# Optimization experiments

Measured on AMD Instinct MI355X. Metric: run time of the kernel, lower is better.

Reference implementation:

```python
import jax, jax.numpy as jnp
import numpy as np

HIDDEN = 2048
KEY_DIM = 2048
NUM_HEADS = 16
EPS = 1e-05


def rms_norm(x, w, eps=EPS):
    ms = jnp.mean(x * x, axis=-1, keepdims=True)
    return x * jax.lax.rsqrt(ms + eps) * w


def setup_inputs() -> dict:
    key = jax.random.key(0)
    ks = jax.random.split(key, 6)
    bound = 1.0 / np.sqrt(HIDDEN)  # kaiming-uniform-ish scale
    x = jax.random.normal(ks[0], (2, 2048, HIDDEN), dtype=jnp.float32)
    rms_w = jnp.ones((HIDDEN,), dtype=jnp.float32)
    Wq = jax.random.uniform(ks[1], (HIDDEN, KEY_DIM), jnp.float32, -bound, bound)
    Wk = jax.random.uniform(ks[2], (HIDDEN, KEY_DIM), jnp.float32, -bound, bound)
    Wv = jax.random.uniform(ks[3], (HIDDEN, KEY_DIM), jnp.float32, -bound, bound)
    Wo = jax.random.uniform(ks[4], (KEY_DIM, HIDDEN), jnp.float32, -bound, bound)
    return {"x": x, "rms_w": rms_w, "Wq": Wq, "Wk": Wk, "Wv": Wv, "Wo": Wo}


def reference(x, rms_w, Wq, Wk, Wv, Wo):
    B, S, _ = x.shape
    residual = x
    xn = rms_norm(x, rms_w)
    # project and split heads: [B,S,H,Dh]
    q = (xn @ Wq).reshape(B, S, NUM_HEADS, KEY_DIM // NUM_HEADS)
    k = (xn @ Wk).reshape(B, S, NUM_HEADS, KEY_DIM // NUM_HEADS)
    v = (xn @ Wv).reshape(B, S, NUM_HEADS, KEY_DIM // NUM_HEADS)
    # NOTE: original scales by 1/sqrt(key_dim), not head_dim — kept faithful
    scale = 1.0 / jnp.sqrt(jnp.float32(KEY_DIM))
    scores = jnp.einsum('bshd,bthd->bhst', q, k) * scale  # [B,H,S,S]
    causal = jnp.tril(jnp.ones((S, S), dtype=bool))
    scores = jnp.where(causal[None, None], scores, -jnp.inf)
    probs = jax.nn.softmax(scores, axis=-1)  # stable max-subtract internally
    out = jnp.einsum('bhst,bthd->bshd', probs, v).reshape(B, S, KEY_DIM)
    return out @ Wo + residual
```

## Files before the change

kernel.cpp:

```cpp
#include <hip/hip_runtime.h>
#include <math.h>

typedef __attribute__((ext_vector_type(8))) short bf16x8;
typedef __attribute__((ext_vector_type(4))) float f32x4;
typedef __attribute__((ext_vector_type(16))) float f32x16;

#define HID 2048
#define SEQ 2048
#define NH  16
#define DH  128
#define QS_LOG2E 0.0318793607f

__device__ __forceinline__ ushort f2bf(float f) {
  union { float f; unsigned u; } v; v.f = f;
  unsigned r = v.u + 0x7fffu + ((v.u >> 16) & 1u);
  return (ushort)(r >> 16);
}

__device__ __forceinline__ void gload16(const ushort* g, ushort* l) {
  __builtin_amdgcn_global_load_lds((const __attribute__((address_space(1))) void*)g,
                                   (__attribute__((address_space(3))) void*)l,
                                   16, 0, 0);
}

#define VMCNT(n) asm volatile("s_waitcnt vmcnt(" #n ")" ::: "memory")
#define ABAR()   asm volatile("s_barrier" ::: "memory")

__global__ __launch_bounds__(256) void k_prep(const float* __restrict__ W0,
                                              const float* __restrict__ W1,
                                              const float* __restrict__ W2,
                                              const float* __restrict__ W3,
                                              ushort* __restrict__ T0,
                                              ushort* __restrict__ T3,
                                              const float* __restrict__ x,
                                              const float* __restrict__ rw,
                                              ushort* __restrict__ xn) {
  const int z = blockIdx.z;
  if (z < 4) {
    __shared__ float t[32][33];
    const float* W = (z == 0) ? W0 : (z == 1) ? W1 : (z == 2) ? W2 : W3;
    ushort* Wt = (z == 3) ? T3 : (T0 + (size_t)z * 2048 * 2048);
    int n0 = blockIdx.x * 32, k0 = blockIdx.y * 32;
    int tx = threadIdx.x, ty = threadIdx.y;
    for (int i = ty; i < 32; i += 8)
      t[i][tx] = W[(size_t)(k0 + i) * HID + n0 + tx];
    __syncthreads();
    for (int i = ty; i < 32; i += 8)
      Wt[(size_t)(n0 + i) * HID + k0 + tx] = f2bf(t[tx][i]);
  } else {
    const int tid = threadIdx.y * 32 + threadIdx.x;
    const int row = blockIdx.y * 64 + blockIdx.x;
    const float* xr = x + (size_t)row * HID;
    int base = tid * 8;
    float4 a = *(const float4*)(xr + base);
    float4 c = *(const float4*)(xr + base + 4);
    float ss = a.x*a.x + a.y*a.y + a.z*a.z + a.w*a.w
             + c.x*c.x + c.y*c.y + c.z*c.z + c.w*c.w;
    #pragma unroll
    for (int off = 32; off > 0; off >>= 1) ss += __shfl_xor(ss, off);
    __shared__ float red[4];
    if ((tid & 63) == 0) red[tid >> 6] = ss;
    __syncthreads();
    float tot = red[0] + red[1] + red[2] + red[3];
    float sc = rsqrtf(tot * (1.0f / HID) + 1e-5f);
    float4 wa = *(const float4*)(rw + base);
    float4 wc = *(const float4*)(rw + base + 4);
    ushort h[8];
    h[0] = f2bf(a.x * sc * wa.x); h[1] = f2bf(a.y * sc * wa.y);
    h[2] = f2bf(a.z * sc * wa.z); h[3] = f2bf(a.w * sc * wa.w);
    h[4] = f2bf(c.x * sc * wc.x); h[5] = f2bf(c.y * sc * wc.y);
    h[6] = f2bf(c.z * sc * wc.z); h[7] = f2bf(c.w * sc * wc.w);
    int4 pk;
    pk.x = h[0] | ((int)h[1] << 16);
    pk.y = h[2] | ((int)h[3] << 16);
    pk.z = h[4] | ((int)h[5] << 16);
    pk.w = h[6] | ((int)h[7] << 16);
    *(int4*)&xn[(size_t)row * HID + base] = pk;
  }
}

__global__ __launch_bounds__(512, 2) void k_gemm10(const ushort* __restrict__ A,
                                                   const ushort* __restrict__ Bt,
                                                   ushort* __restrict__ obf,
                                                   ushort* __restrict__ vt) {
  constexpr int K = 2048;
  __shared__ ushort lds[8][8192];
  const int tid = threadIdx.x;
  const int lane = tid & 63, w = tid >> 6;
  const int wm = w >> 2, wn = w & 3;
  const int g = lane >> 4, l15 = lane & 15;
  const int bm = blockIdx.y, bn = blockIdx.x;

  f32x4 acc[8][4];
  #pragma unroll
  for (int i = 0; i < 8; ++i)
    #pragma unroll
    for (int j = 0; j < 4; ++j) acc[i][j] = f32x4{0.f, 0.f, 0.f, 0.f};

  const ushort* pA[2][2];
  const ushort* pB[2][2];
  #pragma unroll
  for (int kh = 0; kh < 2; ++kh)
    #pragma unroll
    for (int L = 0; L < 2; ++L) {
      int row = L * 128 + w * 16 + (lane >> 2);
      int ck = (lane & 3) ^ ((row >> 1) & 3);
      pA[kh][L] = &A[(size_t)(bm * 256 + row) * K + kh * 32 + ck * 8];
      pB[kh][L] = &Bt[(size_t)(bn * 256 + row) * K + kh * 32 + ck * 8];
    }

  auto STAGE = [&](int buf, int kh) {
    ushort* ra = lds[buf * 4 + kh * 2 + 0];
    ushort* rb = lds[buf * 4 + kh * 2 + 1];
    #pragma unroll
    for (int L = 0; L < 2; ++L) {
      gload16(pA[kh][L], ra + (L * 8 + w) * 512);
      pA[kh][L] += 64;
    }
    #pragma unroll
    for (int L = 0; L < 2; ++L) {
      gload16(pB[kh][L], rb + (L * 8 + w) * 512);
      pB[kh][L] += 64;
    }
  };

  auto COMP = [&](int buf, int kh) {
    const ushort* ra = lds[buf * 4 + kh * 2 + 0];
    const ushort* rb = lds[buf * 4 + kh * 2 + 1];
    bf16x8 aF[8], bF[4];
    #pragma unroll
    for (int i = 0; i < 8; ++i) {
      int row = wm * 128 + i * 16 + l15;
      aF[i] = *(const bf16x8*)&ra[row * 32 + ((g ^ ((row >> 1) & 3)) * 8)];
    }
    #pragma unroll
    for (int j = 0; j < 4; ++j) {
      int row = wn * 64 + j * 16 + l15;
      bF[j] = *(const bf16x8*)&rb[row * 32 + ((g ^ ((row >> 1) & 3)) * 8)];
    }
    __builtin_amdgcn_s_setprio(1);
    #pragma unroll
    for (int i = 0; i < 8; ++i)
      #pragma unroll
      for (int j = 0; j < 4; ++j)
        acc[i][j] = __builtin_amdgcn_mfma_f32_16x16x32_bf16(aF[i], bF[j], acc[i][j], 0, 0, 0);
    __builtin_amdgcn_s_setprio(0);
  };

  STAGE(0, 0); STAGE(0, 1); STAGE(1, 0);

  #pragma unroll 1
  for (int t = 0; t < 30; ++t) {
    const int b = t & 1, nb = b ^ 1;
    VMCNT(8); ABAR();
    STAGE(nb, 1);
    COMP(b, 0);
    VMCNT(8); ABAR();
    STAGE(b, 0);
    COMP(b, 1);
  }
  VMCNT(8); ABAR(); STAGE(1, 1); COMP(0, 0);
  VMCNT(8); ABAR();               COMP(0, 1);
  VMCNT(4); ABAR(); COMP(1, 0);
  VMCNT(0); ABAR(); COMP(1, 1);

  int rbase = bm * 256 + wm * 128 + g * 4;
  int cbase = bn * 256 + wn * 64 + l15;
  if (bn < 16) {
    const float sc = (bn < 8) ? QS_LOG2E : 1.0f;
    #pragma unroll
    for (int i = 0; i < 8; ++i) {
      #pragma unroll
      for (int j = 0; j < 4; ++j) {
        int col = cbase + j * 16;
        #pragma unroll
        for (int r = 0; r < 4; ++r) {
          int row = rbase + i * 16 + r;
          obf[(size_t)row * 4096 + col] = f2bf(acc[i][j][r] * sc);
        }
      }
    }
  } else {
    #pragma unroll
    for (int i = 0; i < 8; ++i) {
      int rowb = rbase + i * 16;
      int b = rowb >> 11, s = rowb & 2047;
      #pragma unroll
      for (int j = 0; j < 4; ++j) {
        int nv = cbase + j * 16 - 4096;
        int h = nv >> 7, d = nv & 127;
        uint lo = (uint)f2bf(acc[i][j][0]) | ((uint)f2bf(acc[i][j][1]) << 16);
        uint hi = (uint)f2bf(acc[i][j][2]) | ((uint)f2bf(acc[i][j][3]) << 16);
        uint2 pk = {lo, hi};
        *(uint2*)&vt[(size_t)((b * NH + h) * DH + d) * SEQ + s] = pk;
      }
    }
  }
}

__global__ __launch_bounds__(256) void k_gemm7o(const ushort* __restrict__ A,
                                                const ushort* __restrict__ Bt,
                                                float* __restrict__ ofl,
                                                const float* __restrict__ resid,
                                                int K) {
  __shared__ ushort sA[128 * 64];
  __shared__ ushort sB[128 * 64];
  const int tid = threadIdx.x;
  const int lane = tid & 63, w = tid >> 6;
  const int wr = w >> 1, wc = w & 1;
  const int bm = blockIdx.y, bn = blockIdx.x;
  const int g = lane >> 4, l15 = lane & 15;
  f32x4 acc[4][4];
  #pragma unroll
  for (int i = 0; i < 4; ++i)
    #pragma unroll
    for (int j = 0; j < 4; ++j) acc[i][j] = f32x4{0.f, 0.f, 0.f, 0.f};

  const ushort* ap[4];
  const ushort* bp[4];
  ushort* la[4];
  ushort* lb[4];
  #pragma unroll
  for (int c = 0; c < 4; ++c) {
    int id = (w * 4 + c) * 64 + lane;
    int r = id >> 3, ck = id & 7;
    int ke = (ck ^ (r & 7)) * 8;
    ap[c] = &A[(size_t)(bm * 128 + r) * K + ke];
    bp[c] = &Bt[(size_t)(bn * 128 + r) * K + ke];
    la[c] = ((ushort*)sA) + (w * 4 + c) * 512;
    lb[c] = ((ushort*)sB) + (w * 4 + c) * 512;
  }

  const int nt = K / 64;
  #pragma unroll 1
  for (int t = 0; t < nt; ++t) {
    #pragma unroll
    for (int c = 0; c < 4; ++c) {
      gload16(ap[c], la[c]);
      gload16(bp[c], lb[c]);
      ap[c] += 64;
      bp[c] += 64;
    }
    __syncthreads();
    #pragma unroll
    for (int kk = 0; kk < 2; ++kk) {
      bf16x8 aF[4], bF[4];
      #pragma unroll
      for (int i = 0; i < 4; ++i) {
        int row = wr * 64 + i * 16 + l15;
        int cp = (kk * 4 + g) ^ (lane & 7);
        aF[i] = *(const bf16x8*)&sA[row * 64 + cp * 8];
      }
      #pragma unroll
      for (int j = 0; j < 4; ++j) {
        int row = wc * 64 + j * 16 + l15;
        int cp = (kk * 4 + g) ^ (lane & 7);
        bF[j] = *(const bf16x8*)&sB[row * 64 + cp * 8];
      }
      #pragma unroll
      for (int i = 0; i < 4; ++i)
        #pragma unroll
        for (int j = 0; j < 4; ++j)
          acc[i][j] = __builtin_amdgcn_mfma_f32_16x16x32_bf16(aF[i], bF[j], acc[i][j], 0, 0, 0);
    }
    __syncthreads();
  }

  int rbase = bm * 128 + wr * 64 + g * 4;
  int cbase = bn * 128 + wc * 64 + l15;
  #pragma unroll
  for (int i = 0; i < 4; ++i) {
    #pragma unroll
    for (int j = 0; j < 4; ++j) {
      int col = cbase + j * 16;
      #pragma unroll
      for (int r = 0; r < 4; ++r) {
        int row = rbase + i * 16 + r;
        ofl[(size_t)row * HID + col] = acc[i][j][r] + resid[(size_t)row * HID + col];
      }
    }
  }
}

__global__ __launch_bounds__(256, 2) void k_attn6(const ushort* __restrict__ qk,
                                                  const ushort* __restrict__ vt,
                                                  ushort* __restrict__ aout) {
  __shared__ ushort sK[2][64 * 128];
  __shared__ ushort sV[2][128 * 64];
  const int tid = threadIdx.x;
  const int lane = tid & 63, w = tid >> 6;
  const int h2 = lane >> 5;
  const int l31 = lane & 31;
  const int bid = blockIdx.x;
  const int t = bid >> 3;
  const int u = t & 31, v = t >> 5;
  const int bh = (bid & 7) + 8 * (u & 3);
  const int qblk = v ? 15 - (u >> 2) : (u >> 2);
  const int b = bh >> 4, hh = bh & 15;
  const int q0w = qblk * 128 + w * 32;

  bf16x8 qf[8];
  {
    const ushort* qbase = qk + (size_t)(b * SEQ + q0w + l31) * 4096 + hh * DH;
    #pragma unroll
    for (int kk = 0; kk < 8; ++kk) qf[kk] = *(const bf16x8*)&qbase[kk * 16 + h2 * 8];
  }

  const ushort* kp[4];
  const ushort* vp[4];
  int lofs[4];
  #pragma unroll
  for (int c = 0; c < 4; ++c) {
    int id = (w * 4 + c) * 64 + lane;
    int kr = id >> 4, ck = id & 15;
    kp[c] = qk + (size_t)(b * SEQ + kr) * 4096 + 2048 + hh * DH + ((ck ^ (kr & 7)) * 8);
    int dr = id >> 3, cv = id & 7;
    vp[c] = vt + (size_t)(bh * DH + dr) * SEQ + ((cv ^ (dr & 7)) * 8);
    lofs[c] = (w * 4 + c) * 512;
  }

  auto STAGE = [&](int buf) {
    #pragma unroll
    for (int c = 0; c < 4; ++c) {
      gload16(kp[c], &sK[buf][0] + lofs[c]);
      gload16(vp[c], &sV[buf][0] + lofs[c]);
      kp[c] += 64 * 4096;
      vp[c] += 64;
    }
  };

  f32x16 accO[4];
  #pragma unroll
  for (int i = 0; i < 4; ++i)
    #pragma unroll
    for (int r = 0; r < 16; ++r) accO[i][r] = 0.f;
  float l_r = 0.f;

  auto COMPUTE = [&](int tt, int buf) {
    const int t0 = tt * 64;
    f32x16 accS[2];
    #pragma unroll
    for (int i = 0; i < 2; ++i)
      #pragma unroll
      for (int r = 0; r < 16; ++r) accS[i][r] = 0.f;
    #pragma unroll
    for (int kt = 0; kt < 2; ++kt) {
      const int row = kt * 32 + l31;
      #pragma unroll
      for (int kk = 0; kk < 8; ++kk) {
        const int cp = (kk * 2 + h2) ^ (lane & 7);
        bf16x8 kf = *(const bf16x8*)&sK[buf][row * 128 + cp * 8];
        accS[kt] = __builtin_amdgcn_mfma_f32_32x32x16_bf16(kf, qf[kk], accS[kt], 0, 0, 0);
      }
    }
    float rs = 0.f;
    if (t0 + 63 <= q0w) {
      #pragma unroll
      for (int kt = 0; kt < 2; ++kt)
        #pragma unroll
        for (int r = 0; r < 16; ++r) {
          float p = __builtin_amdgcn_exp2f(accS[kt][r]);
          rs += p;
          accS[kt][r] = p;
        }
    } else {
      const int qa = q0w + l31;
      #pragma unroll
      for (int kt = 0; kt < 2; ++kt)
        #pragma unroll
        for (int r = 0; r < 16; ++r) {
          int ka = t0 + kt * 32 + (r & 3) + 8 * (r >> 2) + 4 * h2;
          float p = (ka <= qa) ? __builtin_amdgcn_exp2f(accS[kt][r]) : 0.f;
          rs += p;
          accS[kt][r] = p;
        }
    }
    rs += __shfl_xor(rs, 32);
    l_r += rs;

    uint W[2][4][2];
    #pragma unroll
    for (int kt = 0; kt < 2; ++kt)
      #pragma unroll
      for (int bq = 0; bq < 4; ++bq)
        #pragma unroll
        for (int w2 = 0; w2 < 2; ++w2) {
          uint u0 = __float_as_uint(accS[kt][bq * 4 + w2 * 2]);
          uint u1 = __float_as_uint(accS[kt][bq * 4 + w2 * 2 + 1]);
          W[kt][bq][w2] = (u0 >> 16) | (u1 & 0xffff0000u);
        }
    #pragma unroll
    for (int kc = 0; kc < 4; ++kc) {
      const int kt = kc >> 1, pq = kc & 1;
      uint X0 = W[kt][2 * pq][0],     X1 = W[kt][2 * pq][1];
      uint Y0 = W[kt][2 * pq + 1][0], Y1 = W[kt][2 * pq + 1][1];
      uint sx0 = (uint)__shfl_xor((int)X0, 32);
      uint sx1 = (uint)__shfl_xor((int)X1, 32);
      uint sy0 = (uint)__shfl_xor((int)Y0, 32);
      uint sy1 = (uint)__shfl_xor((int)Y1, 32);
      union { uint u[4]; bf16x8 v; } pu;
      pu.u[0] = h2 ? sy0 : X0;
      pu.u[1] = h2 ? sy1 : X1;
      pu.u[2] = h2 ? Y0 : sx0;
      pu.u[3] = h2 ? Y1 : sx1;
      #pragma unroll
      for (int ds = 0; ds < 4; ++ds) {
        const int dr = ds * 32 + l31;
        const int cp = (kc * 2 + h2) ^ (lane & 7);
        bf16x8 vf = *(const bf16x8*)&sV[buf][dr * 64 + cp * 8];
        accO[ds] = __builtin_amdgcn_mfma_f32_32x32x16_bf16(pu.v, vf, accO[ds], 0, 0, 0);
      }
    }
  };

  const int ntile = 2 * qblk + 2;
  STAGE(0);
  #pragma unroll 1
  for (int tt = 0; tt < ntile - 1; ++tt) {
    STAGE((tt + 1) & 1);
    VMCNT(8);
    ABAR();
    if (tt * 64 <= q0w + 31) COMPUTE(tt, tt & 1);
    ABAR();
  }
  VMCNT(0);
  ABAR();
  if ((ntile - 1) * 64 <= q0w + 31) COMPUTE(ntile - 1, (ntile - 1) & 1);

  float linv = 1.f / l_r;
  #pragma unroll
  for (int r = 0; r < 16; ++r) {
    int qrel = (r & 3) + 8 * (r >> 2) + 4 * h2;
    float li = __shfl(linv, qrel);
    #pragma unroll
    for (int ds = 0; ds < 4; ++ds) {
      aout[(size_t)(b * SEQ + q0w + qrel) * HID + hh * DH + ds * 32 + l31] =
          f2bf(accO[ds][r] * li);
    }
  }
}

extern "C" void kernel_launch(void* const* d_in, const int* in_sizes, int n_in,
                              void* d_out, int out_size, void* d_ws, size_t ws_size,
                              hipStream_t stream) {
  const float* x     = (const float*)d_in[0];
  const float* rms_w = (const float*)d_in[1];
  const float* Wq    = (const float*)d_in[2];
  const float* Wk    = (const float*)d_in[3];
  const float* Wv    = (const float*)d_in[4];
  const float* Wo    = (const float*)d_in[5];
  float* out = (float*)d_out;

  char* ws = (char*)d_ws;
  ushort* WqkvT = (ushort*)ws; ws += (size_t)6144 * 2048 * 2;
  ushort* WoT   = (ushort*)ws; ws += (size_t)2048 * 2048 * 2;
  ushort* xn    = (ushort*)ws; ws += (size_t)4096 * 2048 * 2;
  ushort* qkbuf = (ushort*)ws; ws += (size_t)4096 * 4096 * 2;
  ushort* vt    = (ushort*)ws; ws += (size_t)4096 * 2048 * 2;
  ushort* aout  = (ushort*)ws; ws += (size_t)4096 * 2048 * 2;

  k_prep<<<dim3(64, 64, 5), dim3(32, 8), 0, stream>>>(Wq, Wk, Wv, Wo, WqkvT, WoT,
                                                      x, rms_w, xn);

  k_gemm10<<<dim3(24, 16), 512, 0, stream>>>(xn, WqkvT, qkbuf, vt);

  k_attn6<<<512, 256, 0, stream>>>(qkbuf, vt, aout);

  k_gemm7o<<<dim3(16, 32), 256, 0, stream>>>(aout, WoT, out, x, 2048);
}
```

Before: 255.6 us.

## Shrink QKV GEMM tile to 128x128 with four-slot K pipeline

Replaces the 256x256-tile, 512-thread QKV projection GEMM with a 128x128-tile, 256-thread variant. Each K step is 32 wide and staged through a four-slot LDS ring with three stages in flight, instead of double-buffered 64-wide steps. The grid grows from 384 to 1536 blocks, which fills the CUs more evenly and lowers LDS use per block so more blocks can be resident. The cost is lower arithmetic intensity per block and more global/L2 traffic for the A and B tiles.

```diff
diff --git a/kernel.cpp b/kernel.cpp
--- a/kernel.cpp
+++ b/kernel.cpp
@@ -79,97 +79,89 @@
   }
 }
 
-__global__ __launch_bounds__(512, 2) void k_gemm10(const ushort* __restrict__ A,
+__global__ __launch_bounds__(256, 2) void k_gemm12(const ushort* __restrict__ A,
                                                    const ushort* __restrict__ Bt,
                                                    ushort* __restrict__ obf,
                                                    ushort* __restrict__ vt) {
-  constexpr int K = 2048;
-  __shared__ ushort lds[8][8192];
+  constexpr int K = 2048, NR = 64;
+  __shared__ ushort lds[4][8192];
   const int tid = threadIdx.x;
   const int lane = tid & 63, w = tid >> 6;
-  const int wm = w >> 2, wn = w & 3;
+  const int wr = w >> 1, wc = w & 1;
   const int g = lane >> 4, l15 = lane & 15;
   const int bm = blockIdx.y, bn = blockIdx.x;
 
-  f32x4 acc[8][4];
-  #pragma unroll
-  for (int i = 0; i < 8; ++i)
+  f32x4 acc[4][4];
+  #pragma unroll
+  for (int i = 0; i < 4; ++i)
     #pragma unroll
     for (int j = 0; j < 4; ++j) acc[i][j] = f32x4{0.f, 0.f, 0.f, 0.f};
 
-  const ushort* pA[2][2];
-  const ushort* pB[2][2];
-  #pragma unroll
-  for (int kh = 0; kh < 2; ++kh)
+  const ushort* pA[2];
+  const ushort* pB[2];
+  #pragma unroll
+  for (int L = 0; L < 2; ++L) {
+    int row = L * 64 + (tid >> 2);
+    int ck = (tid & 3) ^ ((row >> 1) & 3);
+    pA[L] = &A[(size_t)(bm * 128 + row) * K + ck * 8];
+    pB[L] = &Bt[(size_t)(bn * 128 + row) * K + ck * 8];
+  }
+
+  auto STAGE = [&](int slot) {
+    ushort* base = lds[slot];
     #pragma unroll
     for (int L = 0; L < 2; ++L) {
-      int row = L * 128 + w * 16 + (lane >> 2);
-      int ck = (lane & 3) ^ ((row >> 1) & 3);
-      pA[kh][L] = &A[(size_t)(bm * 256 + row) * K + kh * 32 + ck * 8];
-      pB[kh][L] = &Bt[(size_t)(bn * 256 + row) * K + kh * 32 + ck * 8];
-    }
-
-  auto STAGE = [&](int buf, int kh) {
-    ushort* ra = lds[buf * 4 + kh * 2 + 0];
-    ushort* rb = lds[buf * 4 + kh * 2 + 1];
+      gload16(pA[L], base + L * 2048 + w * 512);
+      pA[L] += 32;
+    }
     #pragma unroll
     for (int L = 0; L < 2; ++L) {
-      gload16(pA[kh][L], ra + (L * 8 + w) * 512);
-      pA[kh][L] += 64;
-    }
-    #pragma unroll
-    for (int L = 0; L < 2; ++L) {
-      gload16(pB[kh][L], rb + (L * 8 + w) * 512);
-      pB[kh][L] += 64;
+      gload16(pB[L], base + 4096 + L * 2048 + w * 512);
+      pB[L] += 32;
     }
   };
 
-  auto COMP = [&](int buf, int kh) {
-    const ushort* ra = lds[buf * 4 + kh * 2 + 0];
-    const ushort* rb = lds[buf * 4 + kh * 2 + 1];
-    bf16x8 aF[8], bF[4];
-    #pragma unroll
-    for (int i = 0; i < 8; ++i) {
-      int row = wm * 128 + i * 16 + l15;
+  auto COMP = [&](int slot) {
+    const ushort* ra = lds[slot];
+    const ushort* rb = ra + 4096;
+    bf16x8 aF[4], bF[4];
+    #pragma unroll
+    for (int i = 0; i < 4; ++i) {
+      int row = wr * 64 + i * 16 + l15;
       aF[i] = *(const bf16x8*)&ra[row * 32 + ((g ^ ((row >> 1) & 3)) * 8)];
     }
     #pragma unroll
     for (int j = 0; j < 4; ++j) {
-      int row = wn * 64 + j * 16 + l15;
+      int row = wc * 64 + j * 16 + l15;
       bF[j] = *(const bf16x8*)&rb[row * 32 + ((g ^ ((row >> 1) & 3)) * 8)];
     }
     __builtin_amdgcn_s_setprio(1);
     #pragma unroll
-    for (int i = 0; i < 8; ++i)
+    for (int i = 0; i < 4; ++i)
       #pragma unroll
       for (int j = 0; j < 4; ++j)
         acc[i][j] = __builtin_amdgcn_mfma_f32_16x16x32_bf16(aF[i], bF[j], acc[i][j], 0, 0, 0);
     __builtin_amdgcn_s_setprio(0);
   };
 
-  STAGE(0, 0); STAGE(0, 1); STAGE(1, 0);
+  STAGE(0); STAGE(1); STAGE(2);
 
   #pragma unroll 1
-  for (int t = 0; t < 30; ++t) {
-    const int b = t & 1, nb = b ^ 1;
+  for (int r = 0; r <= NR - 4; ++r) {
     VMCNT(8); ABAR();
-    STAGE(nb, 1);
-    COMP(b, 0);
-    VMCNT(8); ABAR();
-    STAGE(b, 0);
-    COMP(b, 1);
-  }
-  VMCNT(8); ABAR(); STAGE(1, 1); COMP(0, 0);
-  VMCNT(8); ABAR();               COMP(0, 1);
-  VMCNT(4); ABAR(); COMP(1, 0);
-  VMCNT(0); ABAR(); COMP(1, 1);
-
-  int rbase = bm * 256 + wm * 128 + g * 4;
-  int cbase = bn * 256 + wn * 64 + l15;
-  if (bn < 16) {
-    const float sc = (bn < 8) ? QS_LOG2E : 1.0f;
-    #pragma unroll
-    for (int i = 0; i < 8; ++i) {
+    STAGE((r + 3) & 3);
+    COMP(r & 3);
+  }
+  VMCNT(8); ABAR(); COMP((NR - 3) & 3);
+  VMCNT(4); ABAR(); COMP((NR - 2) & 3);
+  VMCNT(0); ABAR(); COMP((NR - 1) & 3);
+
+  int rbase = bm * 128 + wr * 64 + g * 4;
+  int cbase = bn * 128 + wc * 64 + l15;
+  if (bn < 32) {
+    const float sc = (bn < 16) ? QS_LOG2E : 1.0f;
+    #pragma unroll
+    for (int i = 0; i < 4; ++i) {
       #pragma unroll
       for (int j = 0; j < 4; ++j) {
         int col = cbase + j * 16;
@@ -182,7 +174,7 @@
     }
   } else {
     #pragma unroll
-    for (int i = 0; i < 8; ++i) {
+    for (int i = 0; i < 4; ++i) {
       int rowb = rbase + i * 16;
       int b = rowb >> 11, s = rowb & 2047;
       #pragma unroll
@@ -462,7 +454,7 @@
   k_prep<<<dim3(64, 64, 5), dim3(32, 8), 0, stream>>>(Wq, Wk, Wv, Wo, WqkvT, WoT,
                                                       x, rms_w, xn);
 
-  k_gemm10<<<dim3(24, 16), 512, 0, stream>>>(xn, WqkvT, qkbuf, vt);
+  k_gemm12<<<dim3(48, 32), 256, 0, stream>>>(xn, WqkvT, qkbuf, vt);
 
   k_attn6<<<512, 256, 0, stream>>>(qkbuf, vt, aout);
 
```

After: 254.8 us. No clear change (-0.3%).
